# Optimization experiments

Hardware: AMD Instinct MI355X
Metric: run time of the kernel (lower is better)

## Reference

```python
import jax, jax.numpy as jnp
import numpy as np

L, D, F, H = 6, 512, 2048, 8
DH = D // H
SCALE = DH ** -0.5
B, S = 2, 2048


def _ln(x, w, b):
    m = jnp.mean(x, axis=-1, keepdims=True)
    v = jnp.var(x, axis=-1, keepdims=True)
    return (x - m) * jax.lax.rsqrt(v + 1e-5) * w + b


def setup_inputs() -> dict:
    key = jax.random.key(0)
    ks = jax.random.split(key, 10)
    s = 0.02
    return {
        "x": jax.random.normal(ks[0], (B, S, D), jnp.float32),
        "mask": jnp.zeros((B, 1, 1, S), jnp.float32),
        "ln1_w": jnp.ones((L, D), jnp.float32),
        "ln1_b": jnp.zeros((L, D), jnp.float32),
        "in_w": s * jax.random.normal(ks[1], (L, D, 3 * D), jnp.float32),
        "in_b": jnp.zeros((L, 3 * D), jnp.float32),
        "out_w": s * jax.random.normal(ks[2], (L, D, D), jnp.float32),
        "out_b": jnp.zeros((L, D), jnp.float32),
        "ln2_w": jnp.ones((L, D), jnp.float32),
        "ln2_b": jnp.zeros((L, D), jnp.float32),
        "ffn1_w": s * jax.random.normal(ks[3], (L, D, F), jnp.float32),
        "ffn1_b": jnp.zeros((L, F), jnp.float32),
        "ffn2_w": s * jax.random.normal(ks[4], (L, F, D), jnp.float32),
        "ffn2_b": jnp.zeros((L, D), jnp.float32),
        "norm_w": jnp.ones((D,), jnp.float32),
        "norm_b": jnp.zeros((D,), jnp.float32),
    }


def reference(x, mask, ln1_w, ln1_b, in_w, in_b, out_w, out_b,
              ln2_w, ln2_b, ffn1_w, ffn1_b, ffn2_w, ffn2_b, norm_w, norm_b):
    def step(h, p):
        (l1w, l1b, iw, ib, ow, ob, l2w, l2b, f1w, f1b, f2w, f2b) = p
        # --- self-attention (pre-norm) ---
        y = _ln(h, l1w, l1b)
        proj = y @ iw + ib                       # [B,S,3D]
        q, k, v = jnp.split(proj, 3, axis=-1)    # each [B,S,D]
        q = q.reshape(B, S, H, DH)
        k = k.reshape(B, S, H, DH)
        v = v.reshape(B, S, H, DH)
        dot = jnp.einsum('bqhd,bkhd->bhqk', q * SCALE, k) + mask  # [B,H,S,S]
        att = jax.nn.softmax(dot, axis=-1)
        o = jnp.einsum('bhqk,bkhd->bqhd', att, v).reshape(B, S, D)
        h = o @ ow + ob + h
        # --- FFN (pre-norm) ---
        y = _ln(h, l2w, l2b)
        y = jax.nn.relu(y @ f1w + f1b) @ f2w + f2b
        return h + y, None

    params = (ln1_w, ln1_b, in_w, in_b, out_w, out_b,
              ln2_w, ln2_b, ffn1_w, ffn1_b, ffn2_w, ffn2_b)
    x, _ = jax.lax.scan(step, x, params)
    return _ln(x, norm_w, norm_b)
```

## Files before the change

kernel.cpp:

```cpp
#include <hip/hip_runtime.h>
#include <hip/hip_bf16.h>
#include <stdint.h>


typedef __bf16 bf16x8 __attribute__((ext_vector_type(8)));
typedef __bf16 bf16x4 __attribute__((ext_vector_type(4)));
typedef float f32x4 __attribute__((ext_vector_type(4)));
typedef unsigned short u16;
typedef unsigned short u16x8 __attribute__((ext_vector_type(8)));

#define NB 2
#define NS 2048
#define ND 512
#define NH 8
#define NDH 64
#define NF 2048
#define NL 6
#define NCHUNK 4
#define CK (NS / NCHUNK)
#define LOG2E 1.4426950408889634f
#define QSCALE (0.125f * LOG2E)

#if defined(__has_builtin)
#if __has_builtin(__builtin_amdgcn_global_load_lds)
#define HAVE_GLDS 1
#endif
#endif
#ifndef HAVE_GLDS
#define HAVE_GLDS 0
#endif

#if HAVE_GLDS
__device__ __forceinline__ void glds16(const u16* g, u16* l) {
  __builtin_amdgcn_global_load_lds(
      (const __attribute__((address_space(1))) unsigned int*)g,
      (__attribute__((address_space(3))) unsigned int*)l, 16, 0, 0);
}
#endif

__device__ __forceinline__ u16 f2bf(float f) {
  unsigned u = __float_as_uint(f);
  u += 0x7FFFu + ((u >> 16) & 1u);
  return (u16)(u >> 16);
}

__global__ __launch_bounds__(256) void wcvt_t(const float* __restrict__ src,
                                              u16* __restrict__ dst,
                                              int K, int N) {
  __shared__ float tile[32][33];
  int l = blockIdx.z;
  const float* s = src + (size_t)l * K * N;
  u16* d = dst + (size_t)l * K * N;
  int k0 = blockIdx.y * 32, n0 = blockIdx.x * 32;
  int tx = threadIdx.x, ty = threadIdx.y;
  for (int i = 0; i < 32; i += 8)
    tile[ty + i][tx] = s[(size_t)(k0 + ty + i) * N + n0 + tx];
  __syncthreads();
  for (int i = 0; i < 32; i += 8)
    d[(size_t)(n0 + ty + i) * K + k0 + tx] = f2bf(tile[tx][ty + i]);
}

template <int OUT_BF16>
__global__ __launch_bounds__(256) void ln_k(const float* __restrict__ x,
                                            const float* __restrict__ w,
                                            const float* __restrict__ b,
                                            void* __restrict__ out) {
  int row = blockIdx.x;
  int t = threadIdx.x;
  const float* xr = x + (size_t)row * ND;
  float2 v = ((const float2*)xr)[t];
  float s = v.x + v.y, ss = v.x * v.x + v.y * v.y;
  for (int o = 32; o > 0; o >>= 1) {
    s += __shfl_down(s, o);
    ss += __shfl_down(ss, o);
  }
  __shared__ float rs[4], rss[4];
  if ((t & 63) == 0) { rs[t >> 6] = s; rss[t >> 6] = ss; }
  __syncthreads();
  float S = rs[0] + rs[1] + rs[2] + rs[3];
  float SS = rss[0] + rss[1] + rss[2] + rss[3];
  float mean = S * (1.0f / ND);
  float var = SS * (1.0f / ND) - mean * mean;
  float rstd = rsqrtf(var + 1e-5f);
  float2 wv = ((const float2*)w)[t];
  float2 bv = ((const float2*)b)[t];
  float y0 = (v.x - mean) * rstd * wv.x + bv.x;
  float y1 = (v.y - mean) * rstd * wv.y + bv.y;
  if (OUT_BF16) {
    ushort2 p; p.x = f2bf(y0); p.y = f2bf(y1);
    ((ushort2*)out)[(size_t)row * (ND / 2) + t] = p;
  } else {
    float2 p; p.x = y0; p.y = y1;
    ((float2*)out)[(size_t)row * (ND / 2) + t] = p;
  }
}

template <int EPI, int BM, int BN, int BK>
__global__ __launch_bounds__(256) void gemm_bt(const u16* __restrict__ A,
                                               const u16* __restrict__ Bt,
                                               const float* __restrict__ bias,
                                               const float* __restrict__ resid,
                                               void* __restrict__ C,
                                               int M, int N, int K) {
  constexpr int MT = BM / 32;
  constexpr int NT = BN / 32;
  constexpr int CB = BK / 8;
  constexpr int RPP = 2048 / BK;
  constexpr int AP = BM / RPP;
  constexpr int BP = BN / RPP;
  constexpr int KK = BK / 32;
  __shared__ u16 la[BM * BK];
  __shared__ u16 lb[BN * BK];
  int bm = blockIdx.y, bn = blockIdx.x;
  int t = threadIdx.x;
  int wave = t >> 6, lane = t & 63, quad = lane >> 4, l15 = lane & 15;
  int wm = (wave >> 1) * (BM / 2), wn = (wave & 1) * (BN / 2);
  f32x4 acc[MT][NT] = {};
  int srow = t / CB;
  int scol = ((t % CB) ^ (srow & (CB - 1))) * 8;
  const u16* Ag = A + (size_t)(bm * BM) * K;
  const u16* Bg = Bt + (size_t)(bn * BN) * K;
#if HAVE_GLDS
  u16* laB = la + wave * 512;
  u16* lbB = lb + wave * 512;
#endif
  for (int k0 = 0; k0 < K; k0 += BK) {
    __syncthreads();
#if HAVE_GLDS
#pragma unroll
    for (int g = 0; g < AP; g++)
      glds16(&Ag[(size_t)(srow + g * RPP) * K + k0 + scol], laB + g * 2048);
#pragma unroll
    for (int g = 0; g < BP; g++)
      glds16(&Bg[(size_t)(srow + g * RPP) * K + k0 + scol], lbB + g * 2048);
#else
#pragma unroll
    for (int g = 0; g < AP; g++)
      *(bf16x8*)&la[(srow + g * RPP) * BK + (t % CB) * 8] =
          *(const bf16x8*)&Ag[(size_t)(srow + g * RPP) * K + k0 + scol];
#pragma unroll
    for (int g = 0; g < BP; g++)
      *(bf16x8*)&lb[(srow + g * RPP) * BK + (t % CB) * 8] =
          *(const bf16x8*)&Bg[(size_t)(srow + g * RPP) * K + k0 + scol];
#endif
    __syncthreads();
#pragma unroll
    for (int kk = 0; kk < KK; kk++) {
      bf16x8 af[MT], bfr[NT];
#pragma unroll
      for (int i = 0; i < MT; i++) {
        int row = wm + i * 16 + l15;
        af[i] = *(const bf16x8*)&la[row * BK + ((kk * 4 + quad) ^ (row & (CB - 1))) * 8];
      }
#pragma unroll
      for (int i = 0; i < NT; i++) {
        int row = wn + i * 16 + l15;
        bfr[i] = *(const bf16x8*)&lb[row * BK + ((kk * 4 + quad) ^ (row & (CB - 1))) * 8];
      }
#pragma unroll
      for (int mt = 0; mt < MT; mt++)
#pragma unroll
        for (int nt = 0; nt < NT; nt++)
          acc[mt][nt] = __builtin_amdgcn_mfma_f32_16x16x32_bf16(
              af[mt], bfr[nt], acc[mt][nt], 0, 0, 0);
    }
  }
#pragma unroll
  for (int mt = 0; mt < MT; mt++)
#pragma unroll
    for (int nt = 0; nt < NT; nt++) {
      int col = bn * BN + wn + nt * 16 + l15;
      float bcol = (EPI == 3) ? 0.f : bias[col];
#pragma unroll
      for (int r = 0; r < 4; r++) {
        int row = bm * BM + wm + mt * 16 + quad * 4 + r;
        float v = acc[mt][nt][r] + ((EPI == 3) ? bias[row] : bcol);
        if (EPI == 1) v = fmaxf(v, 0.f);
        if (EPI == 2)
          ((float*)C)[(size_t)row * N + col] = v + resid[(size_t)row * N + col];
        else
          ((u16*)C)[(size_t)row * N + col] = f2bf(v);
      }
    }
}

__global__ __launch_bounds__(256) void attn_k(const u16* __restrict__ qk,
                                              const u16* __restrict__ vt,
                                              const float* __restrict__ mask,
                                              u16* __restrict__ opart,
                                              float* __restrict__ lbuf) {
  __shared__ u16 kt_s[64 * 64];
  __shared__ u16 vt_s[64 * 64];
  __shared__ u16 p_s[4][16 * 64];
  __shared__ float mask_s[CK];
  int bh = blockIdx.y;
  int b = bh >> 3, h = bh & 7;
  int qt = blockIdx.x;
  int c = blockIdx.z;
  int t = threadIdx.x;
  int wave = t >> 6, lane = t & 63, quad = lane >> 4, l15 = lane & 15;

  {
    const float* mrow = mask + b * NS + c * CK;
    mask_s[t] = mrow[t] * LOG2E;
    mask_s[t + 256] = mrow[t + 256] * LOG2E;
  }

  int qrow = qt * 64 + wave * 16 + l15;
  const u16* qbase = qk + ((size_t)(b * NS + qrow)) * (2 * ND) + h * NDH;
  bf16x8 qf[2];
  qf[0] = *(const bf16x8*)&qbase[quad * 8];
  qf[1] = *(const bf16x8*)&qbase[32 + quad * 8];
#pragma unroll
  for (int e = 0; e < 8; e++) {
    qf[0][e] = (__bf16)((float)qf[0][e] * QSCALE);
    qf[1][e] = (__bf16)((float)qf[1][e] * QSCALE);
  }
  bf16x8 ones;
#pragma unroll
  for (int e = 0; e < 8; e++) ones[e] = (__bf16)1.0f;

  f32x4 oacc[4] = {};
  f32x4 ls = {};

  int srow8 = t >> 3;
  int segsw = ((t & 7) ^ ((t >> 3) & 7)) * 8;
  const u16* kg0 = qk + ((size_t)(b * NS + srow8)) * (2 * ND) + ND + h * NDH + segsw;
  const u16* vg0 = vt + ((size_t)(h * NDH + srow8)) * (NB * NS) + b * NS + segsw;
#if HAVE_GLDS
  u16* ktB = kt_s + wave * 512;
  u16* vtB = vt_s + wave * 512;
#endif
  u16* pw = &p_s[wave][0];
  int l7 = l15 & 7;
  for (int kt0 = c * CK; kt0 < (c + 1) * CK; kt0 += 64) {
    __syncthreads();
#if HAVE_GLDS
    glds16(&kg0[(size_t)kt0 * (2 * ND)], ktB);
    glds16(&kg0[(size_t)(kt0 + 32) * (2 * ND)], ktB + 2048);
    glds16(&vg0[kt0], vtB);
    glds16(&vg0[kt0 + (size_t)32 * (NB * NS)], vtB + 2048);
#else
    *(bf16x8*)&kt_s[srow8 * 64 + (t & 7) * 8] =
        *(const bf16x8*)&kg0[(size_t)kt0 * (2 * ND)];
    *(bf16x8*)&kt_s[(srow8 + 32) * 64 + (t & 7) * 8] =
        *(const bf16x8*)&kg0[(size_t)(kt0 + 32) * (2 * ND)];
    *(bf16x8*)&vt_s[srow8 * 64 + (t & 7) * 8] = *(const bf16x8*)&vg0[kt0];
    *(bf16x8*)&vt_s[(srow8 + 32) * 64 + (t & 7) * 8] =
        *(const bf16x8*)&vg0[kt0 + (size_t)32 * (NB * NS)];
#endif
    __syncthreads();
    int ktl = kt0 - c * CK;
    f32x4 sc[4];
#pragma unroll
    for (int nt = 0; nt < 4; nt++)
      sc[nt] = *(const f32x4*)&mask_s[ktl + nt * 16 + quad * 4];
#pragma unroll
    for (int nt = 0; nt < 4; nt++) {
      int row = nt * 16 + l15;
      bf16x8 kf0 = *(const bf16x8*)&kt_s[row * 64 + (quad ^ (row & 7)) * 8];
      bf16x8 kf1 = *(const bf16x8*)&kt_s[row * 64 + ((quad + 4) ^ (row & 7)) * 8];
      sc[nt] = __builtin_amdgcn_mfma_f32_16x16x32_bf16(kf0, qf[0], sc[nt], 0, 0, 0);
      sc[nt] = __builtin_amdgcn_mfma_f32_16x16x32_bf16(kf1, qf[1], sc[nt], 0, 0, 0);
    }
#pragma unroll
    for (int nt = 0; nt < 4; nt++) {
      float2 plo, phi;
      plo.x = __builtin_amdgcn_exp2f(sc[nt][0]);
      plo.y = __builtin_amdgcn_exp2f(sc[nt][1]);
      phi.x = __builtin_amdgcn_exp2f(sc[nt][2]);
      phi.y = __builtin_amdgcn_exp2f(sc[nt][3]);
      __hip_bfloat162 b01 = __float22bfloat162_rn(plo);
      __hip_bfloat162 b23 = __float22bfloat162_rn(phi);
      uint2 pk;
      pk.x = *reinterpret_cast<unsigned int*>(&b01);
      pk.y = *reinterpret_cast<unsigned int*>(&b23);
      int cb = nt * 2 + (quad >> 1);
      int col = ((cb ^ l7) << 3) + (quad & 1) * 4;
      *reinterpret_cast<uint2*>(&pw[l15 * 64 + col]) = pk;
    }
    asm volatile("s_waitcnt lgkmcnt(0)" ::: "memory");
#pragma unroll
    for (int kk = 0; kk < 2; kk++) {
      int cbr = kk * 4 + quad;
      bf16x8 pf = *(const bf16x8*)&pw[l15 * 64 + ((cbr ^ l7) << 3)];
#pragma unroll
      for (int nt = 0; nt < 4; nt++) {
        int row = nt * 16 + l15;
        bf16x8 vf = *(const bf16x8*)&vt_s[row * 64 + ((kk * 4 + quad) ^ (row & 7)) * 8];
        oacc[nt] = __builtin_amdgcn_mfma_f32_16x16x32_bf16(pf, vf, oacc[nt], 0, 0, 0);
      }
      ls = __builtin_amdgcn_mfma_f32_16x16x32_bf16(pf, ones, ls, 0, 0, 0);
    }
  }
  u16* ob = opart + (((size_t)(c * NB * NH + bh) * NS) + qt * 64 + wave * 16) * NDH;
#pragma unroll
  for (int nt = 0; nt < 4; nt++)
#pragma unroll
    for (int r = 0; r < 4; r++)
      ob[(size_t)(quad * 4 + r) * NDH + nt * 16 + l15] = f2bf(oacc[nt][r]);
  if (l15 == 0) {
    size_t li = (size_t)(c * NB * NH + bh) * NS + qt * 64 + wave * 16 + quad * 4;
#pragma unroll
    for (int r = 0; r < 4; r++) lbuf[li + r] = ls[r];
  }
}

__global__ __launch_bounds__(256) void attn_merge(const u16* __restrict__ opart,
                                                  const float* __restrict__ lbuf,
                                                  u16* __restrict__ o) {
  int gt = blockIdx.x * 256 + threadIdx.x;
  int grp = gt & 7;
  int s = (gt >> 3) & (NS - 1);
  int bh = gt >> 14;
  float L = 0.f;
#pragma unroll
  for (int c = 0; c < NCHUNK; c++)
    L += lbuf[(size_t)(c * NB * NH + bh) * NS + s];
  float inv = 1.0f / L;
  float acc[8] = {};
#pragma unroll
  for (int c = 0; c < NCHUNK; c++) {
    bf16x8 ov = *(const bf16x8*)&opart[((size_t)(c * NB * NH + bh) * NS + s) * NDH + grp * 8];
#pragma unroll
    for (int j = 0; j < 8; j++) acc[j] += (float)ov[j];
  }
  u16x8 res;
#pragma unroll
  for (int j = 0; j < 8; j++) res[j] = f2bf(acc[j] * inv);
  int b = bh >> 3, h = bh & 7;
  *(u16x8*)&o[((size_t)(b * NS + s)) * ND + h * NDH + grp * 8] = res;
}

extern "C" void kernel_launch(void* const* d_in, const int* in_sizes, int n_in,
                              void* d_out, int out_size, void* d_ws, size_t ws_size,
                              hipStream_t stream) {
  const float* x = (const float*)d_in[0];
  const float* mask = (const float*)d_in[1];
  const float* ln1w = (const float*)d_in[2];
  const float* ln1b = (const float*)d_in[3];
  const float* in_w = (const float*)d_in[4];
  const float* in_b = (const float*)d_in[5];
  const float* out_w = (const float*)d_in[6];
  const float* out_b = (const float*)d_in[7];
  const float* ln2w = (const float*)d_in[8];
  const float* ln2b = (const float*)d_in[9];
  const float* f1w = (const float*)d_in[10];
  const float* f1b = (const float*)d_in[11];
  const float* f2w = (const float*)d_in[12];
  const float* f2b = (const float*)d_in[13];
  const float* normw = (const float*)d_in[14];
  const float* normb = (const float*)d_in[15];

  char* ws = (char*)d_ws;
  auto carve = [&](size_t bytes) {
    char* p = ws;
    ws += (bytes + 255) & ~(size_t)255;
    return p;
  };
  u16* wq_t = (u16*)carve((size_t)NL * 3 * ND * ND * 2);
  u16* wo_t = (u16*)carve((size_t)NL * ND * ND * 2);
  u16* w1_t = (u16*)carve((size_t)NL * NF * ND * 2);
  u16* w2_t = (u16*)carve((size_t)NL * ND * NF * 2);
  u16* ybuf = (u16*)carve((size_t)NB * NS * ND * 2);
  u16* qk = (u16*)carve((size_t)NB * NS * 2 * ND * 2);
  u16* vtb = (u16*)carve((size_t)ND * NB * NS * 2);
  u16* obuf = (u16*)carve((size_t)NB * NS * ND * 2);
  u16* ubuf = (u16*)carve((size_t)NB * NS * NF * 2);
  float* hA = (float*)carve((size_t)NB * NS * ND * 4);
  float* hB = (float*)carve((size_t)NB * NS * ND * 4);
  float* lbuf = (float*)carve((size_t)NCHUNK * NB * NH * NS * 4);
  u16* opart = ubuf;

  const int M = NB * NS;
  dim3 tb(32, 8);
  wcvt_t<<<dim3(3 * ND / 32, ND / 32, NL), tb, 0, stream>>>(in_w, wq_t, ND, 3 * ND);
  wcvt_t<<<dim3(ND / 32, ND / 32, NL), tb, 0, stream>>>(out_w, wo_t, ND, ND);
  wcvt_t<<<dim3(NF / 32, ND / 32, NL), tb, 0, stream>>>(f1w, w1_t, ND, NF);
  wcvt_t<<<dim3(ND / 32, NF / 32, NL), tb, 0, stream>>>(f2w, w2_t, NF, ND);

  const float* hin = x;
  for (int l = 0; l < NL; l++) {
    ln_k<1><<<M, 256, 0, stream>>>(hin, ln1w + l * ND, ln1b + l * ND, ybuf);
    gemm_bt<0, 64, 128, 128><<<dim3(2 * ND / 128, M / 64), 256, 0, stream>>>(
        ybuf, wq_t + (size_t)l * 3 * ND * ND, in_b + l * 3 * ND, nullptr, qk,
        M, 2 * ND, ND);
    gemm_bt<3, 64, 64, 128><<<dim3(M / 64, ND / 64), 256, 0, stream>>>(
        wq_t + (size_t)l * 3 * ND * ND + (size_t)2 * ND * ND, ybuf,
        in_b + l * 3 * ND + 2 * ND, nullptr, vtb, ND, M, ND);
    attn_k<<<dim3(NS / 64, NB * NH, NCHUNK), 256, 0, stream>>>(
        qk, vtb, mask, opart, lbuf);
    attn_merge<<<(NB * NH * NS * 8) / 256, 256, 0, stream>>>(opart, lbuf, obuf);
    gemm_bt<2, 64, 64, 128><<<dim3(ND / 64, M / 64), 256, 0, stream>>>(
        obuf, wo_t + (size_t)l * ND * ND, out_b + l * ND, hin, hB, M, ND, ND);
    ln_k<1><<<M, 256, 0, stream>>>(hB, ln2w + l * ND, ln2b + l * ND, ybuf);
    gemm_bt<1, 128, 128, 64><<<dim3(NF / 128, M / 128), 256, 0, stream>>>(
        ybuf, w1_t + (size_t)l * NF * ND, f1b + l * NF, nullptr, ubuf, M, NF, ND);
    gemm_bt<2, 64, 64, 128><<<dim3(ND / 64, M / 64), 256, 0, stream>>>(
        ubuf, w2_t + (size_t)l * ND * NF, f2b + l * ND, hB, hA, M, ND, NF);
    hin = hA;
  }
  ln_k<0><<<M, 256, 0, stream>>>(hA, normw, normb, (float*)d_out);
}
```

Before: 798.0 us.

## Double-buffer LDS tiles in GEMM to overlap global loads with MFMA

The bf16 GEMM kernel now holds two LDS buffers for the A and B tiles. It issues the load for the next K-tile right after a single barrier and then computes on the current tile, so global-to-LDS traffic overlaps the MFMA work. This also removes one barrier per K step. The QK projection GEMM's BK drops from 128 to 64, likely to limit the larger LDS footprint. The cost is double the shared memory per block, which can lower occupancy, especially for the 128x128 FFN tile.

```diff
diff --git a/kernel.cpp b/kernel.cpp
--- a/kernel.cpp
+++ b/kernel.cpp
@@ -109,8 +109,8 @@
   constexpr int AP = BM / RPP;
   constexpr int BP = BN / RPP;
   constexpr int KK = BK / 32;
-  __shared__ u16 la[BM * BK];
-  __shared__ u16 lb[BN * BK];
+  __shared__ u16 la[2][BM * BK];
+  __shared__ u16 lb[2][BN * BK];
   int bm = blockIdx.y, bn = blockIdx.x;
   int t = threadIdx.x;
   int wave = t >> 6, lane = t & 63, quad = lane >> 4, l15 = lane & 15;
@@ -120,13 +120,11 @@
   int scol = ((t % CB) ^ (srow & (CB - 1))) * 8;
   const u16* Ag = A + (size_t)(bm * BM) * K;
   const u16* Bg = Bt + (size_t)(bn * BN) * K;
+
+  auto stage = [&](int k0, int buf) {
 #if HAVE_GLDS
-  u16* laB = la + wave * 512;
-  u16* lbB = lb + wave * 512;
-#endif
-  for (int k0 = 0; k0 < K; k0 += BK) {
-    __syncthreads();
-#if HAVE_GLDS
+    u16* laB = &la[buf][0] + wave * 512;
+    u16* lbB = &lb[buf][0] + wave * 512;
 #pragma unroll
     for (int g = 0; g < AP; g++)
       glds16(&Ag[(size_t)(srow + g * RPP) * K + k0 + scol], laB + g * 2048);
@@ -136,26 +134,35 @@
 #else
 #pragma unroll
     for (int g = 0; g < AP; g++)
-      *(bf16x8*)&la[(srow + g * RPP) * BK + (t % CB) * 8] =
+      *(bf16x8*)&la[buf][(srow + g * RPP) * BK + (t % CB) * 8] =
           *(const bf16x8*)&Ag[(size_t)(srow + g * RPP) * K + k0 + scol];
 #pragma unroll
     for (int g = 0; g < BP; g++)
-      *(bf16x8*)&lb[(srow + g * RPP) * BK + (t % CB) * 8] =
+      *(bf16x8*)&lb[buf][(srow + g * RPP) * BK + (t % CB) * 8] =
           *(const bf16x8*)&Bg[(size_t)(srow + g * RPP) * K + k0 + scol];
 #endif
+  };
+
+  stage(0, 0);
+  const int nk = K / BK;
+  int cur = 0;
+  for (int ks = 0; ks < nk; ks++) {
     __syncthreads();
+    if (ks + 1 < nk) stage((ks + 1) * BK, cur ^ 1);
+    const u16* lac = &la[cur][0];
+    const u16* lbc = &lb[cur][0];
 #pragma unroll
     for (int kk = 0; kk < KK; kk++) {
       bf16x8 af[MT], bfr[NT];
 #pragma unroll
       for (int i = 0; i < MT; i++) {
         int row = wm + i * 16 + l15;
-        af[i] = *(const bf16x8*)&la[row * BK + ((kk * 4 + quad) ^ (row & (CB - 1))) * 8];
+        af[i] = *(const bf16x8*)&lac[row * BK + ((kk * 4 + quad) ^ (row & (CB - 1))) * 8];
       }
 #pragma unroll
       for (int i = 0; i < NT; i++) {
         int row = wn + i * 16 + l15;
-        bfr[i] = *(const bf16x8*)&lb[row * BK + ((kk * 4 + quad) ^ (row & (CB - 1))) * 8];
+        bfr[i] = *(const bf16x8*)&lbc[row * BK + ((kk * 4 + quad) ^ (row & (CB - 1))) * 8];
       }
 #pragma unroll
       for (int mt = 0; mt < MT; mt++)
@@ -164,6 +171,7 @@
           acc[mt][nt] = __builtin_amdgcn_mfma_f32_16x16x32_bf16(
               af[mt], bfr[nt], acc[mt][nt], 0, 0, 0);
     }
+    cur ^= 1;
   }
 #pragma unroll
   for (int mt = 0; mt < MT; mt++)
@@ -382,7 +390,7 @@
   const float* hin = x;
   for (int l = 0; l < NL; l++) {
     ln_k<1><<<M, 256, 0, stream>>>(hin, ln1w + l * ND, ln1b + l * ND, ybuf);
-    gemm_bt<0, 64, 128, 128><<<dim3(2 * ND / 128, M / 64), 256, 0, stream>>>(
+    gemm_bt<0, 64, 128, 64><<<dim3(2 * ND / 128, M / 64), 256, 0, stream>>>(
         ybuf, wq_t + (size_t)l * 3 * ND * ND, in_b + l * 3 * ND, nullptr, qk,
         M, 2 * ND, ND);
     gemm_bt<3, 64, 64, 128><<<dim3(M / 64, ND / 64), 256, 0, stream>>>(
```

Measured after the change: 791.1 us. About the same (-0.9%).
